# Performance work log

Hardware: AMD Instinct MI355X
Metric: run time of the kernel (lower is better)

The kernel has to match this reference:

```python
import jax, jax.numpy as jnp
import numpy as np
from jax import lax

HUMAN_CONF = 0.7
IOU_TH = 0.5


def setup_inputs() -> dict:
    key = jax.random.key(0)
    k1, k2 = jax.random.split(key)
    B, Q, C = 16, 2048, 2
    return {
        "human_logits": jax.random.normal(k1, (B, Q, C), dtype=jnp.float32),
        "pred_boxes": jax.random.uniform(k2, (B, Q, 4), dtype=jnp.float32),  # cxcywh in [0,1]
        "img_h": 800,
        "img_w": 1333,
    }


def box_cxcywh_to_xyxy(b):
    cx, cy, w, h = b[..., 0], b[..., 1], b[..., 2], b[..., 3]
    return jnp.stack([cx - 0.5 * w, cy - 0.5 * h, cx + 0.5 * w, cy + 0.5 * h], axis=-1)


def pairwise_iou(b):
    # b: [Q,4] xyxy -> iou: [Q,Q]
    area = jnp.clip(b[:, 2] - b[:, 0], 0) * jnp.clip(b[:, 3] - b[:, 1], 0)
    lt = jnp.maximum(b[:, None, :2], b[None, :, :2])
    rb = jnp.minimum(b[:, None, 2:], b[None, :, 2:])
    wh = jnp.clip(rb - lt, 0)
    inter = wh[..., 0] * wh[..., 1]
    union = area[:, None] + area[None, :] - inter
    return inter / jnp.maximum(union, 1e-9)


def nms_keep(boxes, scores, valid, iou_th):
    # Greedy NMS on one image with fixed shapes; returns keep mask [Q].
    Q = scores.shape[0]
    order = jnp.argsort(jnp.where(valid, -scores, jnp.inf))  # valid boxes first, score desc
    b = boxes[order]
    v = valid[order]
    iou = pairwise_iou(b)                       # [Q,Q]
    idx = jnp.arange(Q)
    sup_mat = (iou > iou_th) & (idx[None, :] > idx[:, None])  # i suppresses later j

    def step(supp, i):
        keep_i = v[i] & jnp.logical_not(supp[i])
        supp = supp | (keep_i & sup_mat[i])
        return supp, keep_i

    _, keep_sorted = lax.scan(step, jnp.zeros(Q, bool), idx)
    return jnp.zeros(Q, bool).at[order].set(keep_sorted)


def reference(human_logits, pred_boxes, img_h, img_w):
    prob = jax.nn.softmax(human_logits, axis=-1)          # [B,Q,C]
    scores = prob.max(axis=-1)                            # [B,Q]
    labels = prob.argmax(axis=-1)                         # [B,Q]
    boxes = box_cxcywh_to_xyxy(pred_boxes)                # [B,Q,4]
    scale = jnp.array([img_w, img_h, img_w, img_h], dtype=boxes.dtype)
    boxes = boxes * scale
    valid = (labels == 0) & (scores >= HUMAN_CONF)
    keep = jax.vmap(lambda b, s, v: nms_keep(b, s, v, IOU_TH))(boxes, scores, valid)
    scores_out = jnp.where(keep, scores, 0.0)
    boxes_out = jnp.where(keep[..., None], boxes, 0.0).astype(jnp.int32)
    return scores_out, boxes_out, keep
```

## Files before the change

kernel.cpp:

```cpp
#include <hip/hip_runtime.h>
#include <math.h>


#define QN   2048
#define NS   1024
#define MATW 17408

__device__ __forceinline__ int rb32(int wb) { return 64 * wb * (33 - wb); }

__device__ __forceinline__ unsigned long long shfl_xor_u64(unsigned long long x, int m) {
    int lo = __shfl_xor((int)(unsigned)(x & 0xffffffffull), m, 64);
    int hi = __shfl_xor((int)(unsigned)(x >> 32), m, 64);
    return ((unsigned long long)(unsigned)hi << 32) | (unsigned)lo;
}

__device__ __forceinline__ unsigned long long score_key(float2 l, int q, bool* valid_out) {
    float mx = fmaxf(l.x, l.y), mn = fminf(l.x, l.y);
    float e = expf(mn - mx);
    float score = 1.0f / (1.0f + e);
    bool valid = (l.x >= l.y) && (score >= 0.7f);
    *valid_out = valid;
    unsigned sbits = valid ? __float_as_uint(score) : 0u;
    return ((unsigned long long)(~sbits) << 32) | (unsigned)q;
}

__global__ __launch_bounds__(1024) void kprep(
    const float* __restrict__ logits, const float* __restrict__ pboxes,
    const int* __restrict__ img_h_p, const int* __restrict__ img_w_p,
    unsigned* __restrict__ wsM, unsigned short* __restrict__ wsidx,
    float* __restrict__ wsoa, unsigned char* __restrict__ wkeep, int B)
{
    __shared__ unsigned long long skey[QN];
    __shared__ unsigned char ssupp[QN];
    __shared__ int sM;

    const int b = blockIdx.x, tid = threadIdx.x, lane = tid & 63;
    const float sw = (float)(*img_w_p), sh = (float)(*img_h_p);

    if (tid == 0) sM = 0;
    __syncthreads();

    const unsigned long long lmask_lt = (1ull << lane) - 1ull;
#pragma unroll
    for (int qq = 0; qq < 2; ++qq) {
        int q = tid + qq * 1024;
        float2 l = ((const float2*)logits)[b * QN + q];
        bool valid;
        unsigned long long key = score_key(l, q, &valid);
        unsigned long long mb = __ballot(valid);
        int base = 0;
        if (lane == 0 && mb) base = atomicAdd(&sM, __popcll(mb));
        base = __shfl(base, 0, 64);
        if (valid) {
            int slot = base + __popcll(mb & lmask_lt);
            if (slot < NS) skey[slot] = key;
        }
    }
    __syncthreads();
    const int M = sM;

    if (M <= NS) {
        unsigned long long v = (tid < M) ? skey[tid] : ~0ull;
        __syncthreads();
#pragma unroll
        for (int k = 2; k <= 64; k <<= 1) {
            bool dir = ((tid & k) == 0);
#pragma unroll
            for (int j = k >> 1; j > 0; j >>= 1) {
                unsigned long long o = shfl_xor_u64(v, j);
                bool takeMin = (dir == ((tid & j) == 0));
                v = ((v < o) == takeMin) ? v : o;
            }
        }
        for (int k = 128; k <= NS; k <<= 1) {
            bool dir = ((tid & k) == 0);
            for (int j = k >> 1; j >= 64; j >>= 1) {
                skey[tid] = v;
                __syncthreads();
                unsigned long long o = skey[tid ^ j];
                bool takeMin = (dir == ((tid & j) == 0));
                v = ((v < o) == takeMin) ? v : o;
                __syncthreads();
            }
#pragma unroll
            for (int j = 32; j > 0; j >>= 1) {
                unsigned long long o = shfl_xor_u64(v, j);
                bool takeMin = (dir == ((tid & j) == 0));
                v = ((v < o) == takeMin) ? v : o;
            }
        }
        int qi = (int)((unsigned)v & 0xffffu);
        wsidx[b * NS + tid] = (unsigned short)qi;
        float x1 = 0.f, y1 = 0.f, x2 = 0.f, y2 = 0.f, ar = 0.f;
        if (tid < M) {
            float4 pb = ((const float4*)pboxes)[b * QN + qi];
            x1 = (pb.x - 0.5f * pb.z) * sw;
            y1 = (pb.y - 0.5f * pb.w) * sh;
            x2 = (pb.x + 0.5f * pb.z) * sw;
            y2 = (pb.y + 0.5f * pb.w) * sh;
            ar = fmaxf(x2 - x1, 0.f) * fmaxf(y2 - y1, 0.f);
        }
        float* soa = wsoa + (long)b * 5 * NS;
        soa[tid] = x1; soa[NS + tid] = y1; soa[2 * NS + tid] = x2;
        soa[3 * NS + tid] = y2; soa[4 * NS + tid] = ar;
        if (tid == 0) wsM[b] = (unsigned)M;
    } else {
        for (int q = tid; q < QN; q += 1024) {
            float2 l = ((const float2*)logits)[b * QN + q];
            bool valid;
            skey[q] = score_key(l, q, &valid);
            wkeep[b * QN + q] = 0;
        }
        __syncthreads();
        for (int k = 2; k <= QN; k <<= 1)
            for (int j = k >> 1; j > 0; j >>= 1) {
                int i = ((tid & ~(j - 1)) << 1) | (tid & (j - 1));
                int p = i | j;
                bool up = ((i & k) == 0);
                unsigned long long a = skey[i], c2 = skey[p];
                if ((a > c2) == up) { skey[i] = c2; skey[p] = a; }
                __syncthreads();
            }
        for (int s = tid; s < M; s += 1024) ssupp[s] = 0;
        __syncthreads();
        for (int i = 0; i < M; ++i) {
            __syncthreads();
            if (ssupp[i]) continue;
            int ia = (unsigned short)(unsigned)skey[i];
            float4 pa = ((const float4*)pboxes)[b * QN + ia];
            float ax1 = (pa.x - 0.5f * pa.z) * sw, ay1 = (pa.y - 0.5f * pa.w) * sh;
            float ax2 = (pa.x + 0.5f * pa.z) * sw, ay2 = (pa.y + 0.5f * pa.w) * sh;
            float areaA = fmaxf(ax2 - ax1, 0.f) * fmaxf(ay2 - ay1, 0.f);
            for (int jj = i + 1 + tid; jj < M; jj += 1024) {
                int jb = (unsigned short)(unsigned)skey[jj];
                float4 pq = ((const float4*)pboxes)[b * QN + jb];
                float bx1 = (pq.x - 0.5f * pq.z) * sw, by1 = (pq.y - 0.5f * pq.w) * sh;
                float bx2 = (pq.x + 0.5f * pq.z) * sw, by2 = (pq.y + 0.5f * pq.w) * sh;
                float ltx = fmaxf(ax1, bx1), lty = fmaxf(ay1, by1);
                float rbx = fminf(ax2, bx2), rby = fminf(ay2, by2);
                float wx = fmaxf(rbx - ltx, 0.f), wy = fmaxf(rby - lty, 0.f);
                float inter = wx * wy;
                float areaB = fmaxf(bx2 - bx1, 0.f) * fmaxf(by2 - by1, 0.f);
                float uni = areaA + areaB - inter;
                if (inter / fmaxf(uni, 1e-9f) > 0.5f) ssupp[jj] = 1;
            }
        }
        __syncthreads();
        for (int s = tid; s < M; s += 1024)
            if (!ssupp[s]) wkeep[b * QN + (unsigned short)(unsigned)skey[s]] = 1;
        if (tid == 0) wsM[b] = (unsigned)M;
    }
}

__global__ __launch_bounds__(1024) void kmat(
    const unsigned* __restrict__ wsM, const float* __restrict__ wsoa,
    unsigned* __restrict__ wmat, int B)
{
    const int b = blockIdx.x % B, slice = blockIdx.x / B;
    const int tid = threadIdx.x, wave = tid >> 6, lane = tid & 63;
    const int M = (int)wsM[b];
    if (M > NS) return;

    __shared__ float sx1[NS], sy1[NS], sx2[NS], sy2[NS], sar[NS];
    const float* soa = wsoa + (long)b * 5 * NS;
    sx1[tid] = soa[tid];          sy1[tid] = soa[NS + tid];
    sx2[tid] = soa[2 * NS + tid]; sy2[tid] = soa[3 * NS + tid];
    sar[tid] = soa[4 * NS + tid];
    __syncthreads();

    unsigned* mat = wmat + (long)b * MATW;
    const int NG = (M + 3) >> 2;
    const int W64 = (M + 63) >> 6;
    for (int gi = slice * 16 + wave; gi < NG; gi += 128) {
        const int g = gi << 2;
        const int nr = min(4, M - g);
        const int wb = g >> 6;
        const int rl = 32 - 2 * wb;
        float ax1[4], ay1[4], ax2[4], ay2[4], aar[4];
        int rbase[4];
#pragma unroll
        for (int r = 0; r < 4; ++r) {
            int i = g + min(r, nr - 1);
            ax1[r] = sx1[i]; ay1[r] = sy1[i];
            ax2[r] = sx2[i]; ay2[r] = sy2[i]; aar[r] = sar[i];
            rbase[r] = rb32(wb) + ((g + r) & 63) * rl;
        }
        for (int w = wb; w < W64; ++w) {
            int j = (w << 6) | lane;
            float bx1 = sx1[j], by1 = sy1[j], bx2 = sx2[j], by2 = sy2[j], bar = sar[j];
#pragma unroll
            for (int r = 0; r < 4; ++r) {
                float ltx = fmaxf(ax1[r], bx1), lty = fmaxf(ay1[r], by1);
                float rbx = fminf(ax2[r], bx2), rby = fminf(ay2[r], by2);
                float wx = fmaxf(rbx - ltx, 0.f), wy = fmaxf(rby - lty, 0.f);
                float inter = wx * wy;
                float uni = aar[r] + bar - inter;
                float iou = inter / fmaxf(uni, 1e-9f);
                bool sup = (iou > 0.5f) && (j > g + r);
                unsigned long long bal = __ballot(sup);
                if (lane == 0 && r < nr)
                    *(unsigned long long*)(mat + rbase[r] + 2 * (w - wb)) = bal;
            }
        }
    }
}

__global__ __launch_bounds__(1024) void kfin(
    const float* __restrict__ logits, const float* __restrict__ pboxes,
    const int* __restrict__ img_h_p, const int* __restrict__ img_w_p,
    const unsigned* __restrict__ wsM, const unsigned short* __restrict__ wsidx,
    const unsigned* __restrict__ wmat, const unsigned char* __restrict__ wkeep,
    float* __restrict__ out, int B)
{
    __shared__ unsigned char keepq[QN];
    __shared__ unsigned skm[32];

    const int b = blockIdx.x, tid = threadIdx.x;
    const float sw = (float)(*img_w_p), sh = (float)(*img_h_p);
    const int M = (int)wsM[b];

    if (M <= NS) {
        keepq[tid] = 0; keepq[tid + 1024] = 0;
        if (tid < 64) {
            if (tid < 32) skm[tid] = 0;
            const unsigned* gm = wmat + (long)b * MATW;
            unsigned rem = 0;
            const int Ms = __builtin_amdgcn_readfirstlane(M);
            const int C = (Ms + 31) >> 5;
            unsigned rcur[32], rnxt[32];
            if (C > 0) {
                int wb = 0, rl = 32;
                int Lc = min(tid, 31);
                int rb0 = ((0 & 1) << 5) * rl + Lc;
#pragma unroll
                for (int t = 0; t < 32; ++t) rcur[t] = gm[rb0 + t * rl];
            }
            for (int c = 0; c < C; ++c) {
                if (c + 1 < C) {
                    int cn = c + 1, wbn = cn >> 1, rln = 32 - 2 * wbn;
                    int Lcn = min(max(tid, 2 * wbn), 31);
                    int rb0n = rb32(wbn) + ((cn & 1) << 5) * rln + (Lcn - 2 * wbn);
#pragma unroll
                    for (int t = 0; t < 32; ++t) rnxt[t] = gm[rb0n + t * rln];
                }
                unsigned rw = (unsigned)__builtin_amdgcn_readlane((int)rem, c);
                unsigned keepmask = 0;
                int lim = min(32, Ms - (c << 5));
#pragma unroll
                for (int t = 0; t < 32; ++t) {
                    if (t < lim && !((rw >> t) & 1u)) {
                        keepmask |= (1u << t);
                        rem |= rcur[t];
                        rw |= (unsigned)__builtin_amdgcn_readlane((int)rcur[t], c);
                    }
                }
                if (tid == 0) skm[c] = keepmask;
                if (c + 1 < C) {
#pragma unroll
                    for (int t = 0; t < 32; ++t) rcur[t] = rnxt[t];
                }
            }
        }
        __syncthreads();
        for (int s = tid; s < M; s += 1024)
            if ((skm[s >> 5] >> (s & 31)) & 1u) keepq[wsidx[b * NS + s]] = 1;
        __syncthreads();
    } else {
        keepq[tid] = wkeep[b * QN + tid];
        keepq[tid + 1024] = wkeep[b * QN + tid + 1024];
        __syncthreads();
    }

    const long BQ = (long)B * QN;
#pragma unroll
    for (int qq = 0; qq < 2; ++qq) {
        int q = tid + qq * 1024;
        int base = b * QN + q;
        float2 l = ((const float2*)logits)[base];
        float e = expf(fminf(l.x, l.y) - fmaxf(l.x, l.y));
        float score = 1.0f / (1.0f + e);
        float4 pb = ((const float4*)pboxes)[base];
        float x1 = (pb.x - 0.5f * pb.z) * sw, y1 = (pb.y - 0.5f * pb.w) * sh;
        float x2 = (pb.x + 0.5f * pb.z) * sw, y2 = (pb.y + 0.5f * pb.w) * sh;
        int kp = keepq[q];
        out[base] = kp ? score : 0.f;
        out[BQ * 5 + base] = kp ? 1.f : 0.f;
        float4 ob;
        ob.x = kp ? truncf(x1) : 0.f;
        ob.y = kp ? truncf(y1) : 0.f;
        ob.z = kp ? truncf(x2) : 0.f;
        ob.w = kp ? truncf(y2) : 0.f;
        ((float4*)(out + BQ))[base] = ob;
    }
}

extern "C" void kernel_launch(void* const* d_in, const int* in_sizes, int n_in,
                              void* d_out, int out_size, void* d_ws, size_t ws_size,
                              hipStream_t stream) {
    const float* logits = (const float*)d_in[0];
    const float* pboxes = (const float*)d_in[1];
    const int*   img_h  = (const int*)d_in[2];
    const int*   img_w  = (const int*)d_in[3];
    float* out = (float*)d_out;
    const int B = in_sizes[0] / (QN * 2);

    char* ws = (char*)d_ws;
    unsigned*       wsM   = (unsigned*)(ws + 0);
    unsigned short* wsidx = (unsigned short*)(ws + 256);
    float*          wsoa  = (float*)(ws + 33024);
    unsigned*       wmat  = (unsigned*)(ws + 360704);
    unsigned char*  wkeep = (unsigned char*)(ws + 1474816);

    kprep<<<dim3(B), dim3(1024), 0, stream>>>(logits, pboxes, img_h, img_w,
                                              wsM, wsidx, wsoa, wkeep, B);
    kmat<<<dim3(B * 8), dim3(1024), 0, stream>>>(wsM, wsoa, wmat, B);
    kfin<<<dim3(B), dim3(1024), 0, stream>>>(logits, pboxes, img_h, img_w,
                                             wsM, wsidx, wmat, wkeep, out, B);
}
```

Baseline: 106.9 us.

## Merge three NMS kernels into one cooperative kernel with grid syncs

```diff
diff --git a/kernel.cpp b/kernel.cpp
--- a/kernel.cpp
+++ b/kernel.cpp
@@ -1,5 +1,8 @@
 #include <hip/hip_runtime.h>
+#include <hip/hip_cooperative_groups.h>
 #include <math.h>
+
+namespace cg = cooperative_groups;
 
 
 #define QN   2048
@@ -24,273 +27,273 @@
     return ((unsigned long long)(~sbits) << 32) | (unsigned)q;
 }
 
-__global__ __launch_bounds__(1024) void kprep(
+__global__ __launch_bounds__(1024) void postproc_coop(
     const float* __restrict__ logits, const float* __restrict__ pboxes,
     const int* __restrict__ img_h_p, const int* __restrict__ img_w_p,
     unsigned* __restrict__ wsM, unsigned short* __restrict__ wsidx,
-    float* __restrict__ wsoa, unsigned char* __restrict__ wkeep, int B)
+    float* __restrict__ wsoa, unsigned* __restrict__ wmat,
+    unsigned char* __restrict__ wkeep, float* __restrict__ out, int B)
 {
-    __shared__ unsigned long long skey[QN];
-    __shared__ unsigned char ssupp[QN];
-    __shared__ int sM;
-
-    const int b = blockIdx.x, tid = threadIdx.x, lane = tid & 63;
+    cg::grid_group grid = cg::this_grid();
+    __shared__ __align__(16) char smem[20608];
+
+    const int blk = blockIdx.x;
+    const int b = blk % B;
+    const int slice = blk / B;
+    const int tid = threadIdx.x, lane = tid & 63, wave = tid >> 6;
     const float sw = (float)(*img_w_p), sh = (float)(*img_h_p);
 
-    if (tid == 0) sM = 0;
-    __syncthreads();
-
-    const unsigned long long lmask_lt = (1ull << lane) - 1ull;
-#pragma unroll
-    for (int qq = 0; qq < 2; ++qq) {
-        int q = tid + qq * 1024;
-        float2 l = ((const float2*)logits)[b * QN + q];
-        bool valid;
-        unsigned long long key = score_key(l, q, &valid);
-        unsigned long long mb = __ballot(valid);
-        int base = 0;
-        if (lane == 0 && mb) base = atomicAdd(&sM, __popcll(mb));
-        base = __shfl(base, 0, 64);
-        if (valid) {
-            int slot = base + __popcll(mb & lmask_lt);
-            if (slot < NS) skey[slot] = key;
-        }
-    }
-    __syncthreads();
-    const int M = sM;
-
-    if (M <= NS) {
-        unsigned long long v = (tid < M) ? skey[tid] : ~0ull;
+    if (slice == 0) {
+        unsigned long long* skey = (unsigned long long*)smem;
+        unsigned char* ssupp = (unsigned char*)(smem + 16384);
+        int* sMp = (int*)(smem + 18432);
+        if (tid == 0) *sMp = 0;
         __syncthreads();
-#pragma unroll
-        for (int k = 2; k <= 64; k <<= 1) {
-            bool dir = ((tid & k) == 0);
-#pragma unroll
-            for (int j = k >> 1; j > 0; j >>= 1) {
-                unsigned long long o = shfl_xor_u64(v, j);
-                bool takeMin = (dir == ((tid & j) == 0));
-                v = ((v < o) == takeMin) ? v : o;
-            }
-        }
-        for (int k = 128; k <= NS; k <<= 1) {
-            bool dir = ((tid & k) == 0);
-            for (int j = k >> 1; j >= 64; j >>= 1) {
-                skey[tid] = v;
-                __syncthreads();
-                unsigned long long o = skey[tid ^ j];
-                bool takeMin = (dir == ((tid & j) == 0));
-                v = ((v < o) == takeMin) ? v : o;
-                __syncthreads();
-            }
-#pragma unroll
-            for (int j = 32; j > 0; j >>= 1) {
-                unsigned long long o = shfl_xor_u64(v, j);
-                bool takeMin = (dir == ((tid & j) == 0));
-                v = ((v < o) == takeMin) ? v : o;
-            }
-        }
-        int qi = (int)((unsigned)v & 0xffffu);
-        wsidx[b * NS + tid] = (unsigned short)qi;
-        float x1 = 0.f, y1 = 0.f, x2 = 0.f, y2 = 0.f, ar = 0.f;
-        if (tid < M) {
-            float4 pb = ((const float4*)pboxes)[b * QN + qi];
-            x1 = (pb.x - 0.5f * pb.z) * sw;
-            y1 = (pb.y - 0.5f * pb.w) * sh;
-            x2 = (pb.x + 0.5f * pb.z) * sw;
-            y2 = (pb.y + 0.5f * pb.w) * sh;
-            ar = fmaxf(x2 - x1, 0.f) * fmaxf(y2 - y1, 0.f);
-        }
-        float* soa = wsoa + (long)b * 5 * NS;
-        soa[tid] = x1; soa[NS + tid] = y1; soa[2 * NS + tid] = x2;
-        soa[3 * NS + tid] = y2; soa[4 * NS + tid] = ar;
-        if (tid == 0) wsM[b] = (unsigned)M;
-    } else {
-        for (int q = tid; q < QN; q += 1024) {
+
+        const unsigned long long lmask_lt = (1ull << lane) - 1ull;
+#pragma unroll
+        for (int qq = 0; qq < 2; ++qq) {
+            int q = tid + qq * 1024;
             float2 l = ((const float2*)logits)[b * QN + q];
             bool valid;
-            skey[q] = score_key(l, q, &valid);
-            wkeep[b * QN + q] = 0;
+            unsigned long long key = score_key(l, q, &valid);
+            unsigned long long mb = __ballot(valid);
+            int base = 0;
+            if (lane == 0 && mb) base = atomicAdd(sMp, __popcll(mb));
+            base = __shfl(base, 0, 64);
+            if (valid) {
+                int slot = base + __popcll(mb & lmask_lt);
+                if (slot < NS) skey[slot] = key;
+            }
         }
         __syncthreads();
-        for (int k = 2; k <= QN; k <<= 1)
-            for (int j = k >> 1; j > 0; j >>= 1) {
-                int i = ((tid & ~(j - 1)) << 1) | (tid & (j - 1));
-                int p = i | j;
-                bool up = ((i & k) == 0);
-                unsigned long long a = skey[i], c2 = skey[p];
-                if ((a > c2) == up) { skey[i] = c2; skey[p] = a; }
+        const int M = *sMp;
+
+        if (M <= NS) {
+            unsigned long long v = (tid < M) ? skey[tid] : ~0ull;
+            __syncthreads();
+#pragma unroll
+            for (int k = 2; k <= 64; k <<= 1) {
+                bool dir = ((tid & k) == 0);
+#pragma unroll
+                for (int j = k >> 1; j > 0; j >>= 1) {
+                    unsigned long long o = shfl_xor_u64(v, j);
+                    bool takeMin = (dir == ((tid & j) == 0));
+                    v = ((v < o) == takeMin) ? v : o;
+                }
+            }
+            for (int k = 128; k <= NS; k <<= 1) {
+                bool dir = ((tid & k) == 0);
+                for (int j = k >> 1; j >= 64; j >>= 1) {
+                    skey[tid] = v;
+                    __syncthreads();
+                    unsigned long long o = skey[tid ^ j];
+                    bool takeMin = (dir == ((tid & j) == 0));
+                    v = ((v < o) == takeMin) ? v : o;
+                    __syncthreads();
+                }
+#pragma unroll
+                for (int j = 32; j > 0; j >>= 1) {
+                    unsigned long long o = shfl_xor_u64(v, j);
+                    bool takeMin = (dir == ((tid & j) == 0));
+                    v = ((v < o) == takeMin) ? v : o;
+                }
+            }
+            int qi = (int)((unsigned)v & 0xffffu);
+            wsidx[b * NS + tid] = (unsigned short)qi;
+            float x1 = 0.f, y1 = 0.f, x2 = 0.f, y2 = 0.f, ar = 0.f;
+            if (tid < M) {
+                float4 pb = ((const float4*)pboxes)[b * QN + qi];
+                x1 = (pb.x - 0.5f * pb.z) * sw;
+                y1 = (pb.y - 0.5f * pb.w) * sh;
+                x2 = (pb.x + 0.5f * pb.z) * sw;
+                y2 = (pb.y + 0.5f * pb.w) * sh;
+                ar = fmaxf(x2 - x1, 0.f) * fmaxf(y2 - y1, 0.f);
+            }
+            float* soa = wsoa + (long)b * 5 * NS;
+            soa[tid] = x1; soa[NS + tid] = y1; soa[2 * NS + tid] = x2;
+            soa[3 * NS + tid] = y2; soa[4 * NS + tid] = ar;
+            if (tid == 0) wsM[b] = (unsigned)M;
+        } else {
+            for (int q = tid; q < QN; q += 1024) {
+                float2 l = ((const float2*)logits)[b * QN + q];
+                bool valid;
+                skey[q] = score_key(l, q, &valid);
+                wkeep[b * QN + q] = 0;
+            }
+            __syncthreads();
+            for (int k = 2; k <= QN; k <<= 1)
+                for (int j = k >> 1; j > 0; j >>= 1) {
+                    int i = ((tid & ~(j - 1)) << 1) | (tid & (j - 1));
+                    int p = i | j;
+                    bool up = ((i & k) == 0);
+                    unsigned long long a = skey[i], c2 = skey[p];
+                    if ((a > c2) == up) { skey[i] = c2; skey[p] = a; }
+                    __syncthreads();
+                }
+            for (int s = tid; s < M; s += 1024) ssupp[s] = 0;
+            __syncthreads();
+            for (int i = 0; i < M; ++i) {
                 __syncthreads();
-            }
-        for (int s = tid; s < M; s += 1024) ssupp[s] = 0;
-        __syncthreads();
-        for (int i = 0; i < M; ++i) {
-            __syncthreads();
-            if (ssupp[i]) continue;
-            int ia = (unsigned short)(unsigned)skey[i];
-            float4 pa = ((const float4*)pboxes)[b * QN + ia];
-            float ax1 = (pa.x - 0.5f * pa.z) * sw, ay1 = (pa.y - 0.5f * pa.w) * sh;
-            float ax2 = (pa.x + 0.5f * pa.z) * sw, ay2 = (pa.y + 0.5f * pa.w) * sh;
-            float areaA = fmaxf(ax2 - ax1, 0.f) * fmaxf(ay2 - ay1, 0.f);
-            for (int jj = i + 1 + tid; jj < M; jj += 1024) {
-                int jb = (unsigned short)(unsigned)skey[jj];
-                float4 pq = ((const float4*)pboxes)[b * QN + jb];
-                float bx1 = (pq.x - 0.5f * pq.z) * sw, by1 = (pq.y - 0.5f * pq.w) * sh;
-                float bx2 = (pq.x + 0.5f * pq.z) * sw, by2 = (pq.y + 0.5f * pq.w) * sh;
-                float ltx = fmaxf(ax1, bx1), lty = fmaxf(ay1, by1);
-                float rbx = fminf(ax2, bx2), rby = fminf(ay2, by2);
-                float wx = fmaxf(rbx - ltx, 0.f), wy = fmaxf(rby - lty, 0.f);
-                float inter = wx * wy;
-                float areaB = fmaxf(bx2 - bx1, 0.f) * fmaxf(by2 - by1, 0.f);
-                float uni = areaA + areaB - inter;
-                if (inter / fmaxf(uni, 1e-9f) > 0.5f) ssupp[jj] = 1;
-            }
-        }
-        __syncthreads();
-        for (int s = tid; s < M; s += 1024)
-            if (!ssupp[s]) wkeep[b * QN + (unsigned short)(unsigned)skey[s]] = 1;
-        if (tid == 0) wsM[b] = (unsigned)M;
+                if (ssupp[i]) continue;
+                int ia = (unsigned short)(unsigned)skey[i];
+                float4 pa = ((const float4*)pboxes)[b * QN + ia];
+                float ax1 = (pa.x - 0.5f * pa.z) * sw, ay1 = (pa.y - 0.5f * pa.w) * sh;
+                float ax2 = (pa.x + 0.5f * pa.z) * sw, ay2 = (pa.y + 0.5f * pa.w) * sh;
+                float areaA = fmaxf(ax2 - ax1, 0.f) * fmaxf(ay2 - ay1, 0.f);
+                for (int jj = i + 1 + tid; jj < M; jj += 1024) {
+                    int jb = (unsigned short)(unsigned)skey[jj];
+                    float4 pq = ((const float4*)pboxes)[b * QN + jb];
+                    float bx1 = (pq.x - 0.5f * pq.z) * sw, by1 = (pq.y - 0.5f * pq.w) * sh;
+                    float bx2 = (pq.x + 0.5f * pq.z) * sw, by2 = (pq.y + 0.5f * pq.w) * sh;
+                    float ltx = fmaxf(ax1, bx1), lty = fmaxf(ay1, by1);
+                    float rbx = fminf(ax2, bx2), rby = fminf(ay2, by2);
+                    float wx = fmaxf(rbx - ltx, 0.f), wy = fmaxf(rby - lty, 0.f);
+                    float inter = wx * wy;
+                    float areaB = fmaxf(bx2 - bx1, 0.f) * fmaxf(by2 - by1, 0.f);
+                    float uni = areaA + areaB - inter;
+                    if (inter / fmaxf(uni, 1e-9f) > 0.5f) ssupp[jj] = 1;
+                }
+            }
+            __syncthreads();
+            for (int s = tid; s < M; s += 1024)
+                if (!ssupp[s]) wkeep[b * QN + (unsigned short)(unsigned)skey[s]] = 1;
+            if (tid == 0) wsM[b] = (unsigned)M;
+        }
     }
-}
-
-__global__ __launch_bounds__(1024) void kmat(
-    const unsigned* __restrict__ wsM, const float* __restrict__ wsoa,
-    unsigned* __restrict__ wmat, int B)
-{
-    const int b = blockIdx.x % B, slice = blockIdx.x / B;
-    const int tid = threadIdx.x, wave = tid >> 6, lane = tid & 63;
-    const int M = (int)wsM[b];
-    if (M > NS) return;
-
-    __shared__ float sx1[NS], sy1[NS], sx2[NS], sy2[NS], sar[NS];
-    const float* soa = wsoa + (long)b * 5 * NS;
-    sx1[tid] = soa[tid];          sy1[tid] = soa[NS + tid];
-    sx2[tid] = soa[2 * NS + tid]; sy2[tid] = soa[3 * NS + tid];
-    sar[tid] = soa[4 * NS + tid];
-    __syncthreads();
-
-    unsigned* mat = wmat + (long)b * MATW;
-    const int NG = (M + 3) >> 2;
-    const int W64 = (M + 63) >> 6;
-    for (int gi = slice * 16 + wave; gi < NG; gi += 128) {
-        const int g = gi << 2;
-        const int nr = min(4, M - g);
-        const int wb = g >> 6;
-        const int rl = 32 - 2 * wb;
-        float ax1[4], ay1[4], ax2[4], ay2[4], aar[4];
-        int rbase[4];
-#pragma unroll
-        for (int r = 0; r < 4; ++r) {
-            int i = g + min(r, nr - 1);
-            ax1[r] = sx1[i]; ay1[r] = sy1[i];
-            ax2[r] = sx2[i]; ay2[r] = sy2[i]; aar[r] = sar[i];
-            rbase[r] = rb32(wb) + ((g + r) & 63) * rl;
-        }
-        for (int w = wb; w < W64; ++w) {
-            int j = (w << 6) | lane;
-            float bx1 = sx1[j], by1 = sy1[j], bx2 = sx2[j], by2 = sy2[j], bar = sar[j];
-#pragma unroll
-            for (int r = 0; r < 4; ++r) {
-                float ltx = fmaxf(ax1[r], bx1), lty = fmaxf(ay1[r], by1);
-                float rbx = fminf(ax2[r], bx2), rby = fminf(ay2[r], by2);
-                float wx = fmaxf(rbx - ltx, 0.f), wy = fmaxf(rby - lty, 0.f);
-                float inter = wx * wy;
-                float uni = aar[r] + bar - inter;
-                float iou = inter / fmaxf(uni, 1e-9f);
-                bool sup = (iou > 0.5f) && (j > g + r);
-                unsigned long long bal = __ballot(sup);
-                if (lane == 0 && r < nr)
-                    *(unsigned long long*)(mat + rbase[r] + 2 * (w - wb)) = bal;
+
+    grid.sync();
+
+    {
+        const int M = (int)wsM[b];
+        if (M <= NS) {
+            float* sx1 = (float*)smem;
+            float* sy1 = (float*)(smem + 4096);
+            float* sx2 = (float*)(smem + 8192);
+            float* sy2 = (float*)(smem + 12288);
+            float* sar = (float*)(smem + 16384);
+            const float* soa = wsoa + (long)b * 5 * NS;
+            sx1[tid] = soa[tid];          sy1[tid] = soa[NS + tid];
+            sx2[tid] = soa[2 * NS + tid]; sy2[tid] = soa[3 * NS + tid];
+            sar[tid] = soa[4 * NS + tid];
+            __syncthreads();
+
+            unsigned* mat = wmat + (long)b * MATW;
+            const int NG = (M + 3) >> 2;
+            const int W64 = (M + 63) >> 6;
+            for (int gi = slice * 16 + wave; gi < NG; gi += 128) {
+                const int g = gi << 2;
+                const int nr = min(4, M - g);
+                const int wb = g >> 6;
+                const int rl = 32 - 2 * wb;
+                float ax1[4], ay1[4], ax2[4], ay2[4], aar[4];
+                int rbase[4];
+#pragma unroll
+                for (int r = 0; r < 4; ++r) {
+                    int i = g + min(r, nr - 1);
+                    ax1[r] = sx1[i]; ay1[r] = sy1[i];
+                    ax2[r] = sx2[i]; ay2[r] = sy2[i]; aar[r] = sar[i];
+                    rbase[r] = rb32(wb) + ((g + r) & 63) * rl;
+                }
+                for (int w = wb; w < W64; ++w) {
+                    int j = (w << 6) | lane;
+                    float bx1 = sx1[j], by1 = sy1[j], bx2 = sx2[j], by2 = sy2[j], bar = sar[j];
+#pragma unroll
+                    for (int r = 0; r < 4; ++r) {
+                        float ltx = fmaxf(ax1[r], bx1), lty = fmaxf(ay1[r], by1);
+                        float rbx = fminf(ax2[r], bx2), rby = fminf(ay2[r], by2);
+                        float wx = fmaxf(rbx - ltx, 0.f), wy = fmaxf(rby - lty, 0.f);
+                        float inter = wx * wy;
+                        float uni = aar[r] + bar - inter;
+                        float iou = inter / fmaxf(uni, 1e-9f);
+                        bool sup = (iou > 0.5f) && (j > g + r);
+                        unsigned long long bal = __ballot(sup);
+                        if (lane == 0 && r < nr)
+                            *(unsigned long long*)(mat + rbase[r] + 2 * (w - wb)) = bal;
+                    }
+                }
             }
         }
     }
-}
-
-__global__ __launch_bounds__(1024) void kfin(
-    const float* __restrict__ logits, const float* __restrict__ pboxes,
-    const int* __restrict__ img_h_p, const int* __restrict__ img_w_p,
-    const unsigned* __restrict__ wsM, const unsigned short* __restrict__ wsidx,
-    const unsigned* __restrict__ wmat, const unsigned char* __restrict__ wkeep,
-    float* __restrict__ out, int B)
-{
-    __shared__ unsigned char keepq[QN];
-    __shared__ unsigned skm[32];
-
-    const int b = blockIdx.x, tid = threadIdx.x;
-    const float sw = (float)(*img_w_p), sh = (float)(*img_h_p);
-    const int M = (int)wsM[b];
-
-    if (M <= NS) {
-        keepq[tid] = 0; keepq[tid + 1024] = 0;
-        if (tid < 64) {
-            if (tid < 32) skm[tid] = 0;
-            const unsigned* gm = wmat + (long)b * MATW;
-            unsigned rem = 0;
-            const int Ms = __builtin_amdgcn_readfirstlane(M);
-            const int C = (Ms + 31) >> 5;
-            unsigned rcur[32], rnxt[32];
-            if (C > 0) {
-                int wb = 0, rl = 32;
-                int Lc = min(tid, 31);
-                int rb0 = ((0 & 1) << 5) * rl + Lc;
-#pragma unroll
-                for (int t = 0; t < 32; ++t) rcur[t] = gm[rb0 + t * rl];
-            }
-            for (int c = 0; c < C; ++c) {
-                if (c + 1 < C) {
-                    int cn = c + 1, wbn = cn >> 1, rln = 32 - 2 * wbn;
-                    int Lcn = min(max(tid, 2 * wbn), 31);
-                    int rb0n = rb32(wbn) + ((cn & 1) << 5) * rln + (Lcn - 2 * wbn);
-#pragma unroll
-                    for (int t = 0; t < 32; ++t) rnxt[t] = gm[rb0n + t * rln];
-                }
-                unsigned rw = (unsigned)__builtin_amdgcn_readlane((int)rem, c);
-                unsigned keepmask = 0;
-                int lim = min(32, Ms - (c << 5));
-#pragma unroll
-                for (int t = 0; t < 32; ++t) {
-                    if (t < lim && !((rw >> t) & 1u)) {
-                        keepmask |= (1u << t);
-                        rem |= rcur[t];
-                        rw |= (unsigned)__builtin_amdgcn_readlane((int)rcur[t], c);
+
+    grid.sync();
+
+    if (slice == 0) {
+        unsigned char* keepq = (unsigned char*)smem;
+        unsigned* skm = (unsigned*)(smem + 2048);
+        const int M = (int)wsM[b];
+
+        if (M <= NS) {
+            keepq[tid] = 0; keepq[tid + 1024] = 0;
+            if (tid < 64) {
+                if (tid < 32) skm[tid] = 0;
+                const unsigned* gm = wmat + (long)b * MATW;
+                unsigned rem = 0;
+                const int Ms = __builtin_amdgcn_readfirstlane(M);
+                const int C = (Ms + 31) >> 5;
+                unsigned rcur[32], rnxt[32];
+                if (C > 0) {
+                    int Lc = min(tid, 31);
+#pragma unroll
+                    for (int t = 0; t < 32; ++t) rcur[t] = gm[Lc + t * 32];
+                }
+                for (int c = 0; c < C; ++c) {
+                    if (c + 1 < C) {
+                        int cn = c + 1, wbn = cn >> 1, rln = 32 - 2 * wbn;
+                        int Lcn = min(max(tid, 2 * wbn), 31);
+                        int rb0n = rb32(wbn) + ((cn & 1) << 5) * rln + (Lcn - 2 * wbn);
+#pragma unroll
+                        for (int t = 0; t < 32; ++t) rnxt[t] = gm[rb0n + t * rln];
                     }
-                }
-                if (tid == 0) skm[c] = keepmask;
-                if (c + 1 < C) {
-#pragma unroll
-                    for (int t = 0; t < 32; ++t) rcur[t] = rnxt[t];
-                }
-            }
-        }
-        __syncthreads();
-        for (int s = tid; s < M; s += 1024)
-            if ((skm[s >> 5] >> (s & 31)) & 1u) keepq[wsidx[b * NS + s]] = 1;
-        __syncthreads();
-    } else {
-        keepq[tid] = wkeep[b * QN + tid];
-        keepq[tid + 1024] = wkeep[b * QN + tid + 1024];
-        __syncthreads();
-    }
-
-    const long BQ = (long)B * QN;
-#pragma unroll
-    for (int qq = 0; qq < 2; ++qq) {
-        int q = tid + qq * 1024;
-        int base = b * QN + q;
-        float2 l = ((const float2*)logits)[base];
-        float e = expf(fminf(l.x, l.y) - fmaxf(l.x, l.y));
-        float score = 1.0f / (1.0f + e);
-        float4 pb = ((const float4*)pboxes)[base];
-        float x1 = (pb.x - 0.5f * pb.z) * sw, y1 = (pb.y - 0.5f * pb.w) * sh;
-        float x2 = (pb.x + 0.5f * pb.z) * sw, y2 = (pb.y + 0.5f * pb.w) * sh;
-        int kp = keepq[q];
-        out[base] = kp ? score : 0.f;
-        out[BQ * 5 + base] = kp ? 1.f : 0.f;
-        float4 ob;
-        ob.x = kp ? truncf(x1) : 0.f;
-        ob.y = kp ? truncf(y1) : 0.f;
-        ob.z = kp ? truncf(x2) : 0.f;
-        ob.w = kp ? truncf(y2) : 0.f;
-        ((float4*)(out + BQ))[base] = ob;
+                    unsigned rw = (unsigned)__builtin_amdgcn_readlane((int)rem, c);
+                    unsigned keepmask = 0;
+                    int lim = min(32, Ms - (c << 5));
+#pragma unroll
+                    for (int t = 0; t < 32; ++t) {
+                        if (t < lim && !((rw >> t) & 1u)) {
+                            keepmask |= (1u << t);
+                            rem |= rcur[t];
+                            rw |= (unsigned)__builtin_amdgcn_readlane((int)rcur[t], c);
+                        }
+                    }
+                    if (tid == 0) skm[c] = keepmask;
+                    if (c + 1 < C) {
+#pragma unroll
+                        for (int t = 0; t < 32; ++t) rcur[t] = rnxt[t];
+                    }
+                }
+            }
+            __syncthreads();
+            for (int s = tid; s < M; s += 1024)
+                if ((skm[s >> 5] >> (s & 31)) & 1u) keepq[wsidx[b * NS + s]] = 1;
+            __syncthreads();
+        } else {
+            keepq[tid] = wkeep[b * QN + tid];
+            keepq[tid + 1024] = wkeep[b * QN + tid + 1024];
+            __syncthreads();
+        }
+
+        const long BQ = (long)B * QN;
+#pragma unroll
+        for (int qq = 0; qq < 2; ++qq) {
+            int q = tid + qq * 1024;
+            int base = b * QN + q;
+            float2 l = ((const float2*)logits)[base];
+            float e = expf(fminf(l.x, l.y) - fmaxf(l.x, l.y));
+            float score = 1.0f / (1.0f + e);
+            float4 pb = ((const float4*)pboxes)[base];
+            float x1 = (pb.x - 0.5f * pb.z) * sw, y1 = (pb.y - 0.5f * pb.w) * sh;
+            float x2 = (pb.x + 0.5f * pb.z) * sw, y2 = (pb.y + 0.5f * pb.w) * sh;
+            int kp = keepq[q];
+            out[base] = kp ? score : 0.f;
+            out[BQ * 5 + base] = kp ? 1.f : 0.f;
+            float4 ob;
+            ob.x = kp ? truncf(x1) : 0.f;
+            ob.y = kp ? truncf(y1) : 0.f;
+            ob.z = kp ? truncf(x2) : 0.f;
+            ob.w = kp ? truncf(y2) : 0.f;
+            ((float4*)(out + BQ))[base] = ob;
+        }
     }
 }
 
@@ -302,7 +305,7 @@
     const int*   img_h  = (const int*)d_in[2];
     const int*   img_w  = (const int*)d_in[3];
     float* out = (float*)d_out;
-    const int B = in_sizes[0] / (QN * 2);
+    int B = in_sizes[0] / (QN * 2);
 
     char* ws = (char*)d_ws;
     unsigned*       wsM   = (unsigned*)(ws + 0);
@@ -311,9 +314,9 @@
     unsigned*       wmat  = (unsigned*)(ws + 360704);
     unsigned char*  wkeep = (unsigned char*)(ws + 1474816);
 
-    kprep<<<dim3(B), dim3(1024), 0, stream>>>(logits, pboxes, img_h, img_w,
-                                              wsM, wsidx, wsoa, wkeep, B);
-    kmat<<<dim3(B * 8), dim3(1024), 0, stream>>>(wsM, wsoa, wmat, B);
-    kfin<<<dim3(B), dim3(1024), 0, stream>>>(logits, pboxes, img_h, img_w,
-                                             wsM, wsidx, wmat, wkeep, out, B);
+    void* args[] = { (void*)&logits, (void*)&pboxes, (void*)&img_h, (void*)&img_w,
+                     (void*)&wsM, (void*)&wsidx, (void*)&wsoa, (void*)&wmat,
+                     (void*)&wkeep, (void*)&out, (void*)&B };
+    hipLaunchCooperativeKernel((void*)postproc_coop, dim3(B * 8), dim3(1024),
+                               args, 0, stream);
 }
```

Result: slower. 139.9 us (+30.9%).

## Fuse prep and IoU-matrix kernels, replace bitonic sort with rank-by-counting

Applied to the files above, without the earlier changes.

```diff
diff --git a/kernel.cpp b/kernel.cpp
--- a/kernel.cpp
+++ b/kernel.cpp
@@ -7,12 +7,6 @@
 #define MATW 17408
 
 __device__ __forceinline__ int rb32(int wb) { return 64 * wb * (33 - wb); }
-
-__device__ __forceinline__ unsigned long long shfl_xor_u64(unsigned long long x, int m) {
-    int lo = __shfl_xor((int)(unsigned)(x & 0xffffffffull), m, 64);
-    int hi = __shfl_xor((int)(unsigned)(x >> 32), m, 64);
-    return ((unsigned long long)(unsigned)hi << 32) | (unsigned)lo;
-}
 
 __device__ __forceinline__ unsigned long long score_key(float2 l, int q, bool* valid_out) {
     float mx = fmaxf(l.x, l.y), mn = fminf(l.x, l.y);
@@ -24,20 +18,28 @@
     return ((unsigned long long)(~sbits) << 32) | (unsigned)q;
 }
 
-__global__ __launch_bounds__(1024) void kprep(
+__global__ __launch_bounds__(1024) void kbuild(
     const float* __restrict__ logits, const float* __restrict__ pboxes,
     const int* __restrict__ img_h_p, const int* __restrict__ img_w_p,
     unsigned* __restrict__ wsM, unsigned short* __restrict__ wsidx,
-    float* __restrict__ wsoa, unsigned char* __restrict__ wkeep, int B)
+    unsigned* __restrict__ wmat, unsigned char* __restrict__ wkeep, int B)
 {
-    __shared__ unsigned long long skey[QN];
-    __shared__ unsigned char ssupp[QN];
-    __shared__ int sM;
-
-    const int b = blockIdx.x, tid = threadIdx.x, lane = tid & 63;
+    __shared__ __align__(16) char smem[30724];
+    unsigned long long* skey = (unsigned long long*)smem;
+    float* sx1 = (float*)(smem + 8192);
+    float* sy1 = (float*)(smem + 12288);
+    float* sx2 = (float*)(smem + 16384);
+    float* sy2 = (float*)(smem + 20480);
+    float* sar = (float*)(smem + 24576);
+    unsigned short* sidxl = (unsigned short*)(smem + 28672);
+    int* sMp = (int*)(smem + 30720);
+
+    const int blk = blockIdx.x;
+    const int b = blk % B, slice = blk / B;
+    const int tid = threadIdx.x, lane = tid & 63, wave = tid >> 6;
     const float sw = (float)(*img_w_p), sh = (float)(*img_h_p);
 
-    if (tid == 0) sM = 0;
+    if (tid == 0) *sMp = 0;
     __syncthreads();
 
     const unsigned long long lmask_lt = (1ull << lane) - 1ull;
@@ -49,7 +51,7 @@
         unsigned long long key = score_key(l, q, &valid);
         unsigned long long mb = __ballot(valid);
         int base = 0;
-        if (lane == 0 && mb) base = atomicAdd(&sM, __popcll(mb));
+        if (lane == 0 && mb) base = atomicAdd(sMp, __popcll(mb));
         base = __shfl(base, 0, 64);
         if (valid) {
             int slot = base + __popcll(mb & lmask_lt);
@@ -57,58 +59,79 @@
         }
     }
     __syncthreads();
-    const int M = sM;
+    const int M = *sMp;
 
     if (M <= NS) {
-        unsigned long long v = (tid < M) ? skey[tid] : ~0ull;
-        __syncthreads();
-#pragma unroll
-        for (int k = 2; k <= 64; k <<= 1) {
-            bool dir = ((tid & k) == 0);
-#pragma unroll
-            for (int j = k >> 1; j > 0; j >>= 1) {
-                unsigned long long o = shfl_xor_u64(v, j);
-                bool takeMin = (dir == ((tid & j) == 0));
-                v = ((v < o) == takeMin) ? v : o;
-            }
-        }
-        for (int k = 128; k <= NS; k <<= 1) {
-            bool dir = ((tid & k) == 0);
-            for (int j = k >> 1; j >= 64; j >>= 1) {
-                skey[tid] = v;
-                __syncthreads();
-                unsigned long long o = skey[tid ^ j];
-                bool takeMin = (dir == ((tid & j) == 0));
-                v = ((v < o) == takeMin) ? v : o;
-                __syncthreads();
-            }
-#pragma unroll
-            for (int j = 32; j > 0; j >>= 1) {
-                unsigned long long o = shfl_xor_u64(v, j);
-                bool takeMin = (dir == ((tid & j) == 0));
-                v = ((v < o) == takeMin) ? v : o;
-            }
-        }
-        int qi = (int)((unsigned)v & 0xffffu);
-        wsidx[b * NS + tid] = (unsigned short)qi;
-        float x1 = 0.f, y1 = 0.f, x2 = 0.f, y2 = 0.f, ar = 0.f;
+        sx1[tid] = 0.f; sy1[tid] = 0.f; sx2[tid] = 0.f; sy2[tid] = 0.f; sar[tid] = 0.f;
+        sidxl[tid] = 0;
+        __syncthreads();
+
         if (tid < M) {
+            unsigned long long my = skey[tid];
+            int r = 0, j = 0;
+            for (; j + 4 <= M; j += 4)
+                r += (int)(skey[j] < my) + (int)(skey[j + 1] < my)
+                   + (int)(skey[j + 2] < my) + (int)(skey[j + 3] < my);
+            for (; j < M; ++j) r += (int)(skey[j] < my);
+            int qi = (int)((unsigned)my & 0xffffu);
             float4 pb = ((const float4*)pboxes)[b * QN + qi];
-            x1 = (pb.x - 0.5f * pb.z) * sw;
-            y1 = (pb.y - 0.5f * pb.w) * sh;
-            x2 = (pb.x + 0.5f * pb.z) * sw;
-            y2 = (pb.y + 0.5f * pb.w) * sh;
-            ar = fmaxf(x2 - x1, 0.f) * fmaxf(y2 - y1, 0.f);
-        }
-        float* soa = wsoa + (long)b * 5 * NS;
-        soa[tid] = x1; soa[NS + tid] = y1; soa[2 * NS + tid] = x2;
-        soa[3 * NS + tid] = y2; soa[4 * NS + tid] = ar;
-        if (tid == 0) wsM[b] = (unsigned)M;
-    } else {
+            float x1 = (pb.x - 0.5f * pb.z) * sw;
+            float y1 = (pb.y - 0.5f * pb.w) * sh;
+            float x2 = (pb.x + 0.5f * pb.z) * sw;
+            float y2 = (pb.y + 0.5f * pb.w) * sh;
+            sx1[r] = x1; sy1[r] = y1; sx2[r] = x2; sy2[r] = y2;
+            sar[r] = fmaxf(x2 - x1, 0.f) * fmaxf(y2 - y1, 0.f);
+            sidxl[r] = (unsigned short)qi;
+        }
+        __syncthreads();
+
+        if (slice == 0) {
+            wsidx[b * NS + tid] = sidxl[tid];
+            if (tid == 0) wsM[b] = (unsigned)M;
+        }
+
+        unsigned* mat = wmat + (long)b * MATW;
+        const int NG = (M + 3) >> 2;
+        const int W64 = (M + 63) >> 6;
+        for (int gi = slice * 16 + wave; gi < NG; gi += 128) {
+            const int g = gi << 2;
+            const int nr = min(4, M - g);
+            const int wb = g >> 6;
+            const int rl = 32 - 2 * wb;
+            float ax1[4], ay1[4], ax2[4], ay2[4], aar[4];
+            int rbase[4];
+#pragma unroll
+            for (int r = 0; r < 4; ++r) {
+                int i = g + min(r, nr - 1);
+                ax1[r] = sx1[i]; ay1[r] = sy1[i];
+                ax2[r] = sx2[i]; ay2[r] = sy2[i]; aar[r] = sar[i];
+                rbase[r] = rb32(wb) + ((g + r) & 63) * rl;
+            }
+            for (int w = wb; w < W64; ++w) {
+                int j = (w << 6) | lane;
+                float bx1 = sx1[j], by1 = sy1[j], bx2 = sx2[j], by2 = sy2[j], bar = sar[j];
+#pragma unroll
+                for (int r = 0; r < 4; ++r) {
+                    float ltx = fmaxf(ax1[r], bx1), lty = fmaxf(ay1[r], by1);
+                    float rbx = fminf(ax2[r], bx2), rby = fminf(ay2[r], by2);
+                    float wx = fmaxf(rbx - ltx, 0.f), wy = fmaxf(rby - lty, 0.f);
+                    float inter = wx * wy;
+                    float uni = aar[r] + bar - inter;
+                    float iou = inter / fmaxf(uni, 1e-9f);
+                    bool sup = (iou > 0.5f) && (j > g + r);
+                    unsigned long long bal = __ballot(sup);
+                    if (lane == 0 && r < nr)
+                        *(unsigned long long*)(mat + rbase[r] + 2 * (w - wb)) = bal;
+                }
+            }
+        }
+    } else if (slice == 0) {
+        unsigned long long* skeyF = (unsigned long long*)smem;
+        unsigned char* ssupp = (unsigned char*)(smem + 16384);
         for (int q = tid; q < QN; q += 1024) {
             float2 l = ((const float2*)logits)[b * QN + q];
             bool valid;
-            skey[q] = score_key(l, q, &valid);
+            skeyF[q] = score_key(l, q, &valid);
             wkeep[b * QN + q] = 0;
         }
         __syncthreads();
@@ -117,8 +140,8 @@
                 int i = ((tid & ~(j - 1)) << 1) | (tid & (j - 1));
                 int p = i | j;
                 bool up = ((i & k) == 0);
-                unsigned long long a = skey[i], c2 = skey[p];
-                if ((a > c2) == up) { skey[i] = c2; skey[p] = a; }
+                unsigned long long a = skeyF[i], c2 = skeyF[p];
+                if ((a > c2) == up) { skeyF[i] = c2; skeyF[p] = a; }
                 __syncthreads();
             }
         for (int s = tid; s < M; s += 1024) ssupp[s] = 0;
@@ -126,13 +149,13 @@
         for (int i = 0; i < M; ++i) {
             __syncthreads();
             if (ssupp[i]) continue;
-            int ia = (unsigned short)(unsigned)skey[i];
+            int ia = (unsigned short)(unsigned)skeyF[i];
             float4 pa = ((const float4*)pboxes)[b * QN + ia];
             float ax1 = (pa.x - 0.5f * pa.z) * sw, ay1 = (pa.y - 0.5f * pa.w) * sh;
             float ax2 = (pa.x + 0.5f * pa.z) * sw, ay2 = (pa.y + 0.5f * pa.w) * sh;
             float areaA = fmaxf(ax2 - ax1, 0.f) * fmaxf(ay2 - ay1, 0.f);
             for (int jj = i + 1 + tid; jj < M; jj += 1024) {
-                int jb = (unsigned short)(unsigned)skey[jj];
+                int jb = (unsigned short)(unsigned)skeyF[jj];
                 float4 pq = ((const float4*)pboxes)[b * QN + jb];
                 float bx1 = (pq.x - 0.5f * pq.z) * sw, by1 = (pq.y - 0.5f * pq.w) * sh;
                 float bx2 = (pq.x + 0.5f * pq.z) * sw, by2 = (pq.y + 0.5f * pq.w) * sh;
@@ -147,65 +170,12 @@
         }
         __syncthreads();
         for (int s = tid; s < M; s += 1024)
-            if (!ssupp[s]) wkeep[b * QN + (unsigned short)(unsigned)skey[s]] = 1;
+            if (!ssupp[s]) wkeep[b * QN + (unsigned short)(unsigned)skeyF[s]] = 1;
         if (tid == 0) wsM[b] = (unsigned)M;
     }
 }
 
-__global__ __launch_bounds__(1024) void kmat(
-    const unsigned* __restrict__ wsM, const float* __restrict__ wsoa,
-    unsigned* __restrict__ wmat, int B)
-{
-    const int b = blockIdx.x % B, slice = blockIdx.x / B;
-    const int tid = threadIdx.x, wave = tid >> 6, lane = tid & 63;
-    const int M = (int)wsM[b];
-    if (M > NS) return;
-
-    __shared__ float sx1[NS], sy1[NS], sx2[NS], sy2[NS], sar[NS];
-    const float* soa = wsoa + (long)b * 5 * NS;
-    sx1[tid] = soa[tid];          sy1[tid] = soa[NS + tid];
-    sx2[tid] = soa[2 * NS + tid]; sy2[tid] = soa[3 * NS + tid];
-    sar[tid] = soa[4 * NS + tid];
-    __syncthreads();
-
-    unsigned* mat = wmat + (long)b * MATW;
-    const int NG = (M + 3) >> 2;
-    const int W64 = (M + 63) >> 6;
-    for (int gi = slice * 16 + wave; gi < NG; gi += 128) {
-        const int g = gi << 2;
-        const int nr = min(4, M - g);
-        const int wb = g >> 6;
-        const int rl = 32 - 2 * wb;
-        float ax1[4], ay1[4], ax2[4], ay2[4], aar[4];
-        int rbase[4];
-#pragma unroll
-        for (int r = 0; r < 4; ++r) {
-            int i = g + min(r, nr - 1);
-            ax1[r] = sx1[i]; ay1[r] = sy1[i];
-            ax2[r] = sx2[i]; ay2[r] = sy2[i]; aar[r] = sar[i];
-            rbase[r] = rb32(wb) + ((g + r) & 63) * rl;
-        }
-        for (int w = wb; w < W64; ++w) {
-            int j = (w << 6) | lane;
-            float bx1 = sx1[j], by1 = sy1[j], bx2 = sx2[j], by2 = sy2[j], bar = sar[j];
-#pragma unroll
-            for (int r = 0; r < 4; ++r) {
-                float ltx = fmaxf(ax1[r], bx1), lty = fmaxf(ay1[r], by1);
-                float rbx = fminf(ax2[r], bx2), rby = fminf(ay2[r], by2);
-                float wx = fmaxf(rbx - ltx, 0.f), wy = fmaxf(rby - lty, 0.f);
-                float inter = wx * wy;
-                float uni = aar[r] + bar - inter;
-                float iou = inter / fmaxf(uni, 1e-9f);
-                bool sup = (iou > 0.5f) && (j > g + r);
-                unsigned long long bal = __ballot(sup);
-                if (lane == 0 && r < nr)
-                    *(unsigned long long*)(mat + rbase[r] + 2 * (w - wb)) = bal;
-            }
-        }
-    }
-}
-
-__global__ __launch_bounds__(1024) void kfin(
+__global__ __launch_bounds__(1024) void kscan(
     const float* __restrict__ logits, const float* __restrict__ pboxes,
     const int* __restrict__ img_h_p, const int* __restrict__ img_w_p,
     const unsigned* __restrict__ wsM, const unsigned short* __restrict__ wsidx,
@@ -229,11 +199,9 @@
             const int C = (Ms + 31) >> 5;
             unsigned rcur[32], rnxt[32];
             if (C > 0) {
-                int wb = 0, rl = 32;
                 int Lc = min(tid, 31);
-                int rb0 = ((0 & 1) << 5) * rl + Lc;
-#pragma unroll
-                for (int t = 0; t < 32; ++t) rcur[t] = gm[rb0 + t * rl];
+#pragma unroll
+                for (int t = 0; t < 32; ++t) rcur[t] = gm[Lc + t * 32];
             }
             for (int c = 0; c < C; ++c) {
                 if (c + 1 < C) {
@@ -307,13 +275,11 @@
     char* ws = (char*)d_ws;
     unsigned*       wsM   = (unsigned*)(ws + 0);
     unsigned short* wsidx = (unsigned short*)(ws + 256);
-    float*          wsoa  = (float*)(ws + 33024);
-    unsigned*       wmat  = (unsigned*)(ws + 360704);
-    unsigned char*  wkeep = (unsigned char*)(ws + 1474816);
-
-    kprep<<<dim3(B), dim3(1024), 0, stream>>>(logits, pboxes, img_h, img_w,
-                                              wsM, wsidx, wsoa, wkeep, B);
-    kmat<<<dim3(B * 8), dim3(1024), 0, stream>>>(wsM, wsoa, wmat, B);
-    kfin<<<dim3(B), dim3(1024), 0, stream>>>(logits, pboxes, img_h, img_w,
-                                             wsM, wsidx, wmat, wkeep, out, B);
-}
+    unsigned*       wmat  = (unsigned*)(ws + 33024);
+    unsigned char*  wkeep = (unsigned char*)(ws + 1147136);
+
+    kbuild<<<dim3(B * 8), dim3(1024), 0, stream>>>(logits, pboxes, img_h, img_w,
+                                                   wsM, wsidx, wmat, wkeep, B);
+    kscan<<<dim3(B), dim3(1024), 0, stream>>>(logits, pboxes, img_h, img_w,
+                                              wsM, wsidx, wmat, wkeep, out, B);
+}
```

Measured after the change: 108.9 us. No clear change (+1.9%).
